# Kernel tuning notes

Measured on AMD Instinct MI355X. Metric: run time of the kernel, lower is better.

Reference implementation:

```python
import jax, jax.numpy as jnp
import numpy as np

DIM = 16      # must equal K*K per the module's reshape structure
K = 4         # kernel_size
HEADS = 8
SCALE = (DIM // HEADS) ** (-0.5)


def setup_inputs() -> dict:
    key = jax.random.key(0)
    k1, k2 = jax.random.split(key)
    x = jax.random.normal(k1, (2, 64, 67, 67), dtype=jnp.float32)
    # torch Linear(dim, 3*dim, bias=False) weight: [3*dim, dim]
    w_qkv = jax.random.normal(k2, (3 * DIM, DIM), dtype=jnp.float32) * 0.1
    return {"x": x, "w_qkv": w_qkv}


def reference(x, w_qkv):
    B, C, H, W = x.shape
    k = K
    Ho, Wo = H - k + 1, W - k + 1          # unfold output grid (stride=1)
    L = Ho * Wo
    # Unfold: patches[b, c, i*k+j, ph, pw] = x[b, c, ph+i, pw+j]
    # (matches torch F.unfold channel ordering c-major, then i, then j)
    patches = jnp.stack(
        [x[:, :, i:i + Ho, j:j + Wo] for i in range(k) for j in range(k)],
        axis=2,
    )  # [B, C, k*k, Ho, Wo]
    seq = L // (k * k)                      # L must be divisible by k*k
    # [B*C*k*k, seq, k*k] -- flatten (Ho,Wo)->L row-major then split into (seq, k*k)
    xu = patches.reshape(B * C * k * k, seq, k * k)
    # tiny attention over each row; feature dim = k*k = DIM
    qkv = xu @ w_qkv.T                      # [N, seq, 3*DIM]
    q, kk_, v = jnp.split(qkv, 3, axis=-1)
    scores = jnp.einsum('nqd,nkd->nqk', q, kk_) * SCALE   # [N, seq, seq]
    attn = jax.nn.softmax(scores, axis=-1)                # dropout = identity (eval)
    ao = jnp.einsum('nqk,nkd->nqd', attn, v)              # [N, seq, DIM]
    ao = ao.reshape(B, C, k, k, Ho, Wo)
    # overlap-add fold back onto the HxW grid
    out = jnp.zeros_like(x)
    for i in range(k):
        for j in range(k):
            out = out.at[:, :, i:Ho + i, j:Wo + j].add(ao[:, :, i, j])
    return out
```

## Files before the change

### kernel.cpp

```cpp
#include <hip/hip_runtime.h>


#define BATCH 2
#define CHAN 64
#define HWDIM 67
#define SEQ 256
#define DIM 16
#define NSEQ 2048
#define PLANE 4096
#define OUT_TOTAL (BATCH * CHAN * HWDIM * HWDIM)
#define ATT_SCALE 0.70710678118654752f
#define LOG2E 1.44269504088896340736f
#define HTILES 17

typedef _Float16 half4 __attribute__((ext_vector_type(4)));
typedef _Float16 half8 __attribute__((ext_vector_type(8)));
typedef float float4v __attribute__((ext_vector_type(4)));
typedef __fp16 fp16x2 __attribute__((ext_vector_type(2)));
typedef unsigned int uint2v __attribute__((ext_vector_type(2)));

static __device__ __forceinline__ half4 mk_half4(float a, float b, float c, float d) {
    fp16x2 lo = __builtin_amdgcn_cvt_pkrtz(a, b);
    fp16x2 hi = __builtin_amdgcn_cvt_pkrtz(c, d);
    uint2v u;
    u[0] = __builtin_bit_cast(unsigned int, lo);
    u[1] = __builtin_bit_cast(unsigned int, hi);
    return __builtin_bit_cast(half4, u);
}

static __device__ __forceinline__ half4 pack4(float4v c) {
    return mk_half4(c[0], c[1], c[2], c[3]);
}

static __device__ __forceinline__ void att_step(const half4 vf, const float4v sfr,
                                                float& l, float4v& oacc) {
    const float p0 = __builtin_amdgcn_exp2f(sfr[0]);
    const float p1 = __builtin_amdgcn_exp2f(sfr[1]);
    const float p2 = __builtin_amdgcn_exp2f(sfr[2]);
    const float p3 = __builtin_amdgcn_exp2f(sfr[3]);
    l += (p0 + p1) + (p2 + p3);
    const half4 pb = mk_half4(p0, p1, p2, p3);
    oacc = __builtin_amdgcn_mfma_f32_16x16x16f16(vf, pb, oacc, 0, 0, 0);
}

__global__ __launch_bounds__(512, 6) void ska_attn_pass1(
    const float* __restrict__ x,
    const float* __restrict__ w,
    _Float16* __restrict__ ao)
{
    __shared__ __align__(16) _Float16 buf[16][64][8];

    const int n = (int)(blockIdx.x & 7) * 256 + (int)(blockIdx.x >> 3);

    const int p  = n & 15;
    const int bc = n >> 4;
    const int oi = p >> 2;
    const int oj = p & 3;

    const int tid  = threadIdx.x;
    const int wave = tid >> 6;
    const int lane = tid & 63;
    const int o = lane & 15;
    const int g = lane >> 4;

    const float4 wq4 = *(const float4*)(w + ( 0 + o) * DIM + 4 * g);
    const float4 wk4 = *(const float4*)(w + (16 + o) * DIM + 4 * g);
    const float4 wv4 = *(const float4*)(w + (32 + o) * DIM + 4 * g);
    const half4 wqf = mk_half4(wq4.x * (ATT_SCALE * LOG2E), wq4.y * (ATT_SCALE * LOG2E),
                               wq4.z * (ATT_SCALE * LOG2E), wq4.w * (ATT_SCALE * LOG2E));
    const half4 wkf = mk_half4(wk4.x, wk4.y, wk4.z, wk4.w);
    const half4 wvf = mk_half4(wv4.x, wv4.y, wv4.z, wv4.w);

    const float4v zf = (float4v){0.f, 0.f, 0.f, 0.f};

    const int rowbase = bc * (HWDIM * HWDIM) + oi * HWDIM + oj;
    const int col = (o & 3) * 16 + 4 * g;
    half4 qfr[2];
#pragma unroll
    for (int u = 0; u < 2; ++u) {
        const int t = 2 * wave + u;
        const float* xp = x + rowbase + (4 * t + (o >> 2)) * HWDIM + col;
        const half4 xf = mk_half4(xp[0], xp[1], xp[2], xp[3]);
        const half4 kf = pack4(__builtin_amdgcn_mfma_f32_16x16x16f16(wkf, xf, zf, 0, 0, 0));
        const half4 vf = pack4(__builtin_amdgcn_mfma_f32_16x16x16f16(xf, wvf, zf, 0, 0, 0));
        const half8 kv = __builtin_shufflevector(kf, vf, 0, 1, 2, 3, 4, 5, 6, 7);
        *(half8*)&buf[t][lane][0] = kv;
        qfr[u] = pack4(__builtin_amdgcn_mfma_f32_16x16x16f16(wqf, xf, zf, 0, 0, 0));
    }
    __syncthreads();

    float4v oacc0 = zf, oacc1 = zf;
    float l0 = 0.f, l1 = 0.f;

    half8 kvc = *(const half8*)&buf[0][lane][0];
#pragma unroll 4
    for (int t = 0; t < 16; ++t) {
        const half8 kvn = *(const half8*)&buf[(t + 1) & 15][lane][0];
        const half4 kf = __builtin_shufflevector(kvc, kvc, 0, 1, 2, 3);
        const half4 vf = __builtin_shufflevector(kvc, kvc, 4, 5, 6, 7);
        const float4v s0 = __builtin_amdgcn_mfma_f32_16x16x16f16(kf, qfr[0], zf, 0, 0, 0);
        const float4v s1 = __builtin_amdgcn_mfma_f32_16x16x16f16(kf, qfr[1], zf, 0, 0, 0);
        att_step(vf, s0, l0, oacc0);
        att_step(vf, s1, l1, oacc1);
        kvc = kvn;
    }

#pragma unroll
    for (int j = 0; j < 2; ++j) {
        float lj = j ? l1 : l0;
        lj += __shfl_xor(lj, 16, 64);
        lj += __shfl_xor(lj, 32, 64);
        const float rl = __builtin_amdgcn_rcpf(lj);
        const float4v oa = j ? oacc1 : oacc0;
        const int query = (2 * wave + j) * 16 + o;
        const half4 hv = mk_half4(oa[0] * rl, oa[1] * rl,
                                  oa[2] * rl, oa[3] * rl);
        *(half4*)(ao + (size_t)n * PLANE + query * DIM + 4 * g) = hv;
    }
}

__global__ __launch_bounds__(256) void ska_fold_pass2(
    const _Float16* __restrict__ ao,
    float* __restrict__ out)
{
    __shared__ __align__(16) _Float16 sA[16][4][64];

    const int blk = (int)(blockIdx.x & 7) * 272 + (int)(blockIdx.x >> 3);
    const int h0  = (blk % HTILES) * 4;
    const int bc  = blk / HTILES;
    const int tid = threadIdx.x;

    {
        const int pl = tid >> 4;
        const int hh = (tid >> 2) & 3;
        const int pw = (tid & 3) * 16;
        const int i  = pl >> 2;
        const int prow = h0 + hh - i;
        half8 v0, v1;
        if (prow >= 0 && prow < 64) {
            const _Float16* src = ao + ((size_t)(bc * 16 + pl)) * PLANE + prow * 64 + pw;
            v0 = *(const half8*)src;
            v1 = *(const half8*)(src + 8);
        } else {
            const half8 z = (half8)(_Float16)0.f;
            v0 = z; v1 = z;
        }
        *(half8*)&sA[pl][hh][pw]     = v0;
        *(half8*)&sA[pl][hh][pw + 8] = v1;
    }
    __syncthreads();

    for (int px = tid; px < 4 * HWDIM; px += 256) {
        const int hh = px / HWDIM;
        const int ww = px % HWDIM;
        const int h  = h0 + hh;
        if (h >= HWDIM) continue;
        float acc = 0.f;
#pragma unroll
        for (int i = 0; i < 4; ++i) {
#pragma unroll
            for (int j = 0; j < 4; ++j) {
                const int pw = ww - j;
                if (pw < 0 || pw >= 64) continue;
                acc += (float)sA[i * 4 + j][hh][pw];
            }
        }
        out[((size_t)bc * HWDIM + h) * HWDIM + ww] = acc;
    }
}

__global__ __launch_bounds__(256) void ska_attn_atomic(
    const float* __restrict__ x, const float* __restrict__ w,
    float* __restrict__ out)
{
    __shared__ float sw[3 * DIM * DIM];
    __shared__ float sk[SEQ][DIM];
    __shared__ float sv[SEQ][DIM];

    const int n = blockIdx.x, p = n & 15, bc = n >> 4, oi = p >> 2, oj = p & 3;
    const int s = threadIdx.x, ph = s >> 2, pw0 = (s & 3) * DIM;

#pragma unroll
    for (int r = 0; r < 3; ++r) sw[r * 256 + s] = w[r * 256 + s];

    const float* xrow = x + ((size_t)bc * HWDIM + (ph + oi)) * HWDIM + pw0 + oj;
    float xr[DIM];
#pragma unroll
    for (int d = 0; d < DIM; ++d) xr[d] = xrow[d];
    __syncthreads();

    float q[DIM];
#pragma unroll
    for (int o = 0; o < DIM; ++o) {
        float aq = 0.f, ak = 0.f, av = 0.f;
#pragma unroll
        for (int d = 0; d < DIM; ++d) {
            aq += xr[d] * sw[o * DIM + d];
            ak += xr[d] * sw[(DIM + o) * DIM + d];
            av += xr[d] * sw[(2 * DIM + o) * DIM + d];
        }
        q[o] = aq * ATT_SCALE; sk[s][o] = ak; sv[s][o] = av;
    }
    __syncthreads();

    float l = 0.f, acc[DIM];
#pragma unroll
    for (int d = 0; d < DIM; ++d) acc[d] = 0.f;
    for (int t = 0; t < SEQ; ++t) {
        float sc = 0.f;
#pragma unroll
        for (int d = 0; d < DIM; ++d) sc += q[d] * sk[t][d];
        const float pe = __expf(sc);
        l += pe;
#pragma unroll
        for (int d = 0; d < DIM; ++d) acc[d] += pe * sv[t][d];
    }
    const float rl = 1.f / l;
    float* obase = out + ((size_t)bc * HWDIM + (ph + oi)) * HWDIM + pw0 + oj;
#pragma unroll
    for (int d = 0; d < DIM; ++d) atomicAdd(&obase[d], acc[d] * rl);
}

extern "C" void kernel_launch(void* const* d_in, const int* in_sizes, int n_in,
                              void* d_out, int out_size, void* d_ws, size_t ws_size,
                              hipStream_t stream) {
    const float* x = (const float*)d_in[0];
    const float* w = (const float*)d_in[1];
    float* out = (float*)d_out;

    const size_t need = (size_t)NSEQ * PLANE * sizeof(_Float16);
    if (ws_size >= need) {
        _Float16* ao = (_Float16*)d_ws;
        ska_attn_pass1<<<NSEQ, 512, 0, stream>>>(x, w, ao);
        ska_fold_pass2<<<BATCH * CHAN * HTILES, 256, 0, stream>>>(ao, out);
    } else {
        (void)hipMemsetAsync(out, 0, (size_t)out_size * sizeof(float), stream);
        ska_attn_atomic<<<NSEQ, 256, 0, stream>>>(x, w, out);
    }
}
```

Measured before the change: 88.89 us.

## Process four oj sequences per block with double-buffered K/V and prefetched x rows

Each pass-1 block now handles the four sequences that share the same (bc, oi) and differ only by column offset oj, looping over them instead of launching one block per sequence. The x loads for the next sequence are issued before the attention loop, and K/V go into a double-buffered shared array, so one barrier per iteration suffices and global load latency can overlap the MFMA work. Grid size drops by four and the launch bound's minimum-blocks hint goes from 6 to 2. The trade-off is fewer blocks for latency hiding, twice the shared memory per block, and longer serial work per block.

```diff
diff --git a/kernel.cpp b/kernel.cpp
--- a/kernel.cpp
+++ b/kernel.cpp
@@ -43,19 +43,17 @@
     oacc = __builtin_amdgcn_mfma_f32_16x16x16f16(vf, pb, oacc, 0, 0, 0);
 }
 
-__global__ __launch_bounds__(512, 6) void ska_attn_pass1(
+__global__ __launch_bounds__(512, 2) void ska_attn_pass1(
     const float* __restrict__ x,
     const float* __restrict__ w,
     _Float16* __restrict__ ao)
 {
-    __shared__ __align__(16) _Float16 buf[16][64][8];
-
-    const int n = (int)(blockIdx.x & 7) * 256 + (int)(blockIdx.x >> 3);
-
-    const int p  = n & 15;
-    const int bc = n >> 4;
-    const int oi = p >> 2;
-    const int oj = p & 3;
+    __shared__ __align__(16) _Float16 buf[2][16][64][8];
+
+    const int b  = (int)(blockIdx.x & 7) * 64 + (int)(blockIdx.x >> 3);
+    const int bc = b >> 2;
+    const int oi = b & 3;
+    const int n0 = bc * 16 + oi * 4;
 
     const int tid  = threadIdx.x;
     const int wave = tid >> 6;
@@ -73,49 +71,74 @@
 
     const float4v zf = (float4v){0.f, 0.f, 0.f, 0.f};
 
-    const int rowbase = bc * (HWDIM * HWDIM) + oi * HWDIM + oj;
-    const int col = (o & 3) * 16 + 4 * g;
-    half4 qfr[2];
-#pragma unroll
-    for (int u = 0; u < 2; ++u) {
-        const int t = 2 * wave + u;
-        const float* xp = x + rowbase + (4 * t + (o >> 2)) * HWDIM + col;
-        const half4 xf = mk_half4(xp[0], xp[1], xp[2], xp[3]);
-        const half4 kf = pack4(__builtin_amdgcn_mfma_f32_16x16x16f16(wkf, xf, zf, 0, 0, 0));
-        const half4 vf = pack4(__builtin_amdgcn_mfma_f32_16x16x16f16(xf, wvf, zf, 0, 0, 0));
-        const half8 kv = __builtin_shufflevector(kf, vf, 0, 1, 2, 3, 4, 5, 6, 7);
-        *(half8*)&buf[t][lane][0] = kv;
-        qfr[u] = pack4(__builtin_amdgcn_mfma_f32_16x16x16f16(wqf, xf, zf, 0, 0, 0));
-    }
-    __syncthreads();
-
-    float4v oacc0 = zf, oacc1 = zf;
-    float l0 = 0.f, l1 = 0.f;
-
-    half8 kvc = *(const half8*)&buf[0][lane][0];
+    const float* xb = x + ((size_t)bc * HWDIM + oi) * HWDIM + (o & 3) * 16 + 4 * g;
+    const int roff0 = (8 * wave + (o >> 2)) * HWDIM;
+    const int roff1 = roff0 + 4 * HWDIM;
+
+    float xr0a = xb[roff0 + 0], xr0b = xb[roff0 + 1],
+          xr0c = xb[roff0 + 2], xr0d = xb[roff0 + 3];
+    float xr1a = xb[roff1 + 0], xr1b = xb[roff1 + 1],
+          xr1c = xb[roff1 + 2], xr1d = xb[roff1 + 3];
+
+    for (int sq = 0; sq < 4; ++sq) {
+        const int cur = sq & 1;
+
+        half4 qfr0, qfr1;
+        {
+            const half4 xf0 = mk_half4(xr0a, xr0b, xr0c, xr0d);
+            const half4 kf0 = pack4(__builtin_amdgcn_mfma_f32_16x16x16f16(wkf, xf0, zf, 0, 0, 0));
+            const half4 vf0 = pack4(__builtin_amdgcn_mfma_f32_16x16x16f16(xf0, wvf, zf, 0, 0, 0));
+            *(half8*)&buf[cur][2 * wave][lane][0] =
+                __builtin_shufflevector(kf0, vf0, 0, 1, 2, 3, 4, 5, 6, 7);
+            qfr0 = pack4(__builtin_amdgcn_mfma_f32_16x16x16f16(wqf, xf0, zf, 0, 0, 0));
+
+            const half4 xf1 = mk_half4(xr1a, xr1b, xr1c, xr1d);
+            const half4 kf1 = pack4(__builtin_amdgcn_mfma_f32_16x16x16f16(wkf, xf1, zf, 0, 0, 0));
+            const half4 vf1 = pack4(__builtin_amdgcn_mfma_f32_16x16x16f16(xf1, wvf, zf, 0, 0, 0));
+            *(half8*)&buf[cur][2 * wave + 1][lane][0] =
+                __builtin_shufflevector(kf1, vf1, 0, 1, 2, 3, 4, 5, 6, 7);
+            qfr1 = pack4(__builtin_amdgcn_mfma_f32_16x16x16f16(wqf, xf1, zf, 0, 0, 0));
+        }
+
+        if (sq < 3) {
+            const int d = sq + 1;
+            xr0a = xb[roff0 + d + 0]; xr0b = xb[roff0 + d + 1];
+            xr0c = xb[roff0 + d + 2]; xr0d = xb[roff0 + d + 3];
+            xr1a = xb[roff1 + d + 0]; xr1b = xb[roff1 + d + 1];
+            xr1c = xb[roff1 + d + 2]; xr1d = xb[roff1 + d + 3];
+        }
+
+        __syncthreads();
+
+        float4v oacc0 = zf, oacc1 = zf;
+        float l0 = 0.f, l1 = 0.f;
+
+        half8 kvc = *(const half8*)&buf[cur][0][lane][0];
 #pragma unroll 4
-    for (int t = 0; t < 16; ++t) {
-        const half8 kvn = *(const half8*)&buf[(t + 1) & 15][lane][0];
-        const half4 kf = __builtin_shufflevector(kvc, kvc, 0, 1, 2, 3);
-        const half4 vf = __builtin_shufflevector(kvc, kvc, 4, 5, 6, 7);
-        const float4v s0 = __builtin_amdgcn_mfma_f32_16x16x16f16(kf, qfr[0], zf, 0, 0, 0);
-        const float4v s1 = __builtin_amdgcn_mfma_f32_16x16x16f16(kf, qfr[1], zf, 0, 0, 0);
-        att_step(vf, s0, l0, oacc0);
-        att_step(vf, s1, l1, oacc1);
-        kvc = kvn;
-    }
-
-#pragma unroll
-    for (int j = 0; j < 2; ++j) {
-        float lj = j ? l1 : l0;
-        lj += __shfl_xor(lj, 16, 64);
-        lj += __shfl_xor(lj, 32, 64);
-        const float rl = __builtin_amdgcn_rcpf(lj);
-        const float4v oa = j ? oacc1 : oacc0;
-        const int query = (2 * wave + j) * 16 + o;
-        const half4 hv = mk_half4(oa[0] * rl, oa[1] * rl,
-                                  oa[2] * rl, oa[3] * rl);
-        *(half4*)(ao + (size_t)n * PLANE + query * DIM + 4 * g) = hv;
+        for (int t = 0; t < 16; ++t) {
+            const half8 kvn = *(const half8*)&buf[cur][(t + 1) & 15][lane][0];
+            const half4 kf = __builtin_shufflevector(kvc, kvc, 0, 1, 2, 3);
+            const half4 vf = __builtin_shufflevector(kvc, kvc, 4, 5, 6, 7);
+            const float4v s0 = __builtin_amdgcn_mfma_f32_16x16x16f16(kf, qfr0, zf, 0, 0, 0);
+            const float4v s1 = __builtin_amdgcn_mfma_f32_16x16x16f16(kf, qfr1, zf, 0, 0, 0);
+            att_step(vf, s0, l0, oacc0);
+            att_step(vf, s1, l1, oacc1);
+            kvc = kvn;
+        }
+
+        const int n = n0 + sq;
+#pragma unroll
+        for (int j = 0; j < 2; ++j) {
+            float lj = j ? l1 : l0;
+            lj += __shfl_xor(lj, 16, 64);
+            lj += __shfl_xor(lj, 32, 64);
+            const float rl = __builtin_amdgcn_rcpf(lj);
+            const float4v oa = j ? oacc1 : oacc0;
+            const int query = (2 * wave + j) * 16 + o;
+            const half4 hv = mk_half4(oa[0] * rl, oa[1] * rl,
+                                      oa[2] * rl, oa[3] * rl);
+            *(half4*)(ao + (size_t)n * PLANE + query * DIM + 4 * g) = hv;
+        }
     }
 }
 
@@ -231,7 +254,7 @@
     const size_t need = (size_t)NSEQ * PLANE * sizeof(_Float16);
     if (ws_size >= need) {
         _Float16* ao = (_Float16*)d_ws;
-        ska_attn_pass1<<<NSEQ, 512, 0, stream>>>(x, w, ao);
+        ska_attn_pass1<<<NSEQ / 4, 512, 0, stream>>>(x, w, ao);
         ska_fold_pass2<<<BATCH * CHAN * HTILES, 256, 0, stream>>>(ao, out);
     } else {
         (void)hipMemsetAsync(out, 0, (size_t)out_size * sizeof(float), stream);
```

After: 91.37 us. +2.8%, slower.

## Fuse attention and overlap-add fold into one kernel per channel plane

Applied to the files above, without the earlier changes.

Replaces the two-pass pipeline (attention writing fp16 outputs to workspace, then a separate fold kernel) with a single kernel per (batch, channel) plane. Each of 16 waves handles one unfold offset, keeps all K/Q/V fragments in registers, and accumulates normalized outputs into a shared-memory fold buffer with LDS atomics before writing the plane. This removes the global intermediate round trip and a launch. In exchange, the grid shrinks to 128 large blocks, leaving many CUs idle, and register pressure per wave rises.

```diff
diff --git a/kernel.cpp b/kernel.cpp
--- a/kernel.cpp
+++ b/kernel.cpp
@@ -6,12 +6,8 @@
 #define HWDIM 67
 #define SEQ 256
 #define DIM 16
-#define NSEQ 2048
-#define PLANE 4096
-#define OUT_TOTAL (BATCH * CHAN * HWDIM * HWDIM)
 #define ATT_SCALE 0.70710678118654752f
 #define LOG2E 1.44269504088896340736f
-#define HTILES 17
 
 typedef _Float16 half4 __attribute__((ext_vector_type(4)));
 typedef _Float16 half8 __attribute__((ext_vector_type(8)));
@@ -43,22 +39,24 @@
     oacc = __builtin_amdgcn_mfma_f32_16x16x16f16(vf, pb, oacc, 0, 0, 0);
 }
 
-__global__ __launch_bounds__(512, 6) void ska_attn_pass1(
+__global__ __launch_bounds__(1024, 1) void ska_fused(
     const float* __restrict__ x,
     const float* __restrict__ w,
-    _Float16* __restrict__ ao)
+    float* __restrict__ out)
 {
-    __shared__ __align__(16) _Float16 buf[16][64][8];
+    __shared__ float fold[HWDIM][68];
 
-    const int n = (int)(blockIdx.x & 7) * 256 + (int)(blockIdx.x >> 3);
+    const int bc  = blockIdx.x;
+    const int tid = threadIdx.x;
 
-    const int p  = n & 15;
-    const int bc = n >> 4;
-    const int oi = p >> 2;
-    const int oj = p & 3;
+    {
+        float* ff = &fold[0][0];
+        for (int i = tid; i < HWDIM * 68; i += 1024) ff[i] = 0.f;
+    }
 
-    const int tid  = threadIdx.x;
-    const int wave = tid >> 6;
+    const int wv   = tid >> 6;
+    const int ii   = wv >> 2;
+    const int jj   = wv & 3;
     const int lane = tid & 63;
     const int o = lane & 15;
     const int g = lane >> 4;
@@ -73,152 +71,52 @@
 
     const float4v zf = (float4v){0.f, 0.f, 0.f, 0.f};
 
-    const int rowbase = bc * (HWDIM * HWDIM) + oi * HWDIM + oj;
-    const int col = (o & 3) * 16 + 4 * g;
-    half4 qfr[2];
+    const float* xb = x + ((size_t)bc * HWDIM + ii) * HWDIM + (o & 3) * 16 + 4 * g + jj;
+    half4 kf[16], vf[16], qf[16];
 #pragma unroll
-    for (int u = 0; u < 2; ++u) {
-        const int t = 2 * wave + u;
-        const float* xp = x + rowbase + (4 * t + (o >> 2)) * HWDIM + col;
+    for (int t = 0; t < 16; ++t) {
+        const float* xp = xb + (4 * t + (o >> 2)) * HWDIM;
         const half4 xf = mk_half4(xp[0], xp[1], xp[2], xp[3]);
-        const half4 kf = pack4(__builtin_amdgcn_mfma_f32_16x16x16f16(wkf, xf, zf, 0, 0, 0));
-        const half4 vf = pack4(__builtin_amdgcn_mfma_f32_16x16x16f16(xf, wvf, zf, 0, 0, 0));
-        const half8 kv = __builtin_shufflevector(kf, vf, 0, 1, 2, 3, 4, 5, 6, 7);
-        *(half8*)&buf[t][lane][0] = kv;
-        qfr[u] = pack4(__builtin_amdgcn_mfma_f32_16x16x16f16(wqf, xf, zf, 0, 0, 0));
+        kf[t] = pack4(__builtin_amdgcn_mfma_f32_16x16x16f16(wkf, xf, zf, 0, 0, 0));
+        vf[t] = pack4(__builtin_amdgcn_mfma_f32_16x16x16f16(xf, wvf, zf, 0, 0, 0));
+        qf[t] = pack4(__builtin_amdgcn_mfma_f32_16x16x16f16(wqf, xf, zf, 0, 0, 0));
     }
+
     __syncthreads();
 
-    float4v oacc0 = zf, oacc1 = zf;
-    float l0 = 0.f, l1 = 0.f;
-
-    half8 kvc = *(const half8*)&buf[0][lane][0];
-#pragma unroll 4
-    for (int t = 0; t < 16; ++t) {
-        const half8 kvn = *(const half8*)&buf[(t + 1) & 15][lane][0];
-        const half4 kf = __builtin_shufflevector(kvc, kvc, 0, 1, 2, 3);
-        const half4 vf = __builtin_shufflevector(kvc, kvc, 4, 5, 6, 7);
-        const float4v s0 = __builtin_amdgcn_mfma_f32_16x16x16f16(kf, qfr[0], zf, 0, 0, 0);
-        const float4v s1 = __builtin_amdgcn_mfma_f32_16x16x16f16(kf, qfr[1], zf, 0, 0, 0);
-        att_step(vf, s0, l0, oacc0);
-        att_step(vf, s1, l1, oacc1);
-        kvc = kvn;
+#pragma unroll
+    for (int jq = 0; jq < 16; jq += 2) {
+        float4v oacc0 = zf, oacc1 = zf;
+        float l0 = 0.f, l1 = 0.f;
+#pragma unroll
+        for (int t = 0; t < 16; ++t) {
+            const float4v s0 = __builtin_amdgcn_mfma_f32_16x16x16f16(kf[t], qf[jq],     zf, 0, 0, 0);
+            const float4v s1 = __builtin_amdgcn_mfma_f32_16x16x16f16(kf[t], qf[jq + 1], zf, 0, 0, 0);
+            att_step(vf[t], s0, l0, oacc0);
+            att_step(vf[t], s1, l1, oacc1);
+        }
+#pragma unroll
+        for (int u = 0; u < 2; ++u) {
+            float lj = u ? l1 : l0;
+            lj += __shfl_xor(lj, 16, 64);
+            lj += __shfl_xor(lj, 32, 64);
+            const float rl = __builtin_amdgcn_rcpf(lj);
+            const float4v oa = u ? oacc1 : oacc0;
+            const int r = 4 * (jq + u) + (o >> 2) + ii;
+            const int c = 16 * (o & 3) + 4 * g + jj;
+            atomicAdd(&fold[r][c + 0], oa[0] * rl);
+            atomicAdd(&fold[r][c + 1], oa[1] * rl);
+            atomicAdd(&fold[r][c + 2], oa[2] * rl);
+            atomicAdd(&fold[r][c + 3], oa[3] * rl);
+        }
     }
 
-#pragma unroll
-    for (int j = 0; j < 2; ++j) {
-        float lj = j ? l1 : l0;
-        lj += __shfl_xor(lj, 16, 64);
-        lj += __shfl_xor(lj, 32, 64);
-        const float rl = __builtin_amdgcn_rcpf(lj);
-        const float4v oa = j ? oacc1 : oacc0;
-        const int query = (2 * wave + j) * 16 + o;
-        const half4 hv = mk_half4(oa[0] * rl, oa[1] * rl,
-                                  oa[2] * rl, oa[3] * rl);
-        *(half4*)(ao + (size_t)n * PLANE + query * DIM + 4 * g) = hv;
-    }
-}
-
-__global__ __launch_bounds__(256) void ska_fold_pass2(
-    const _Float16* __restrict__ ao,
-    float* __restrict__ out)
-{
-    __shared__ __align__(16) _Float16 sA[16][4][64];
-
-    const int blk = (int)(blockIdx.x & 7) * 272 + (int)(blockIdx.x >> 3);
-    const int h0  = (blk % HTILES) * 4;
-    const int bc  = blk / HTILES;
-    const int tid = threadIdx.x;
-
-    {
-        const int pl = tid >> 4;
-        const int hh = (tid >> 2) & 3;
-        const int pw = (tid & 3) * 16;
-        const int i  = pl >> 2;
-        const int prow = h0 + hh - i;
-        half8 v0, v1;
-        if (prow >= 0 && prow < 64) {
-            const _Float16* src = ao + ((size_t)(bc * 16 + pl)) * PLANE + prow * 64 + pw;
-            v0 = *(const half8*)src;
-            v1 = *(const half8*)(src + 8);
-        } else {
-            const half8 z = (half8)(_Float16)0.f;
-            v0 = z; v1 = z;
-        }
-        *(half8*)&sA[pl][hh][pw]     = v0;
-        *(half8*)&sA[pl][hh][pw + 8] = v1;
-    }
     __syncthreads();
 
-    for (int px = tid; px < 4 * HWDIM; px += 256) {
-        const int hh = px / HWDIM;
-        const int ww = px % HWDIM;
-        const int h  = h0 + hh;
-        if (h >= HWDIM) continue;
-        float acc = 0.f;
-#pragma unroll
-        for (int i = 0; i < 4; ++i) {
-#pragma unroll
-            for (int j = 0; j < 4; ++j) {
-                const int pw = ww - j;
-                if (pw < 0 || pw >= 64) continue;
-                acc += (float)sA[i * 4 + j][hh][pw];
-            }
-        }
-        out[((size_t)bc * HWDIM + h) * HWDIM + ww] = acc;
+    float* ob = out + (size_t)bc * (HWDIM * HWDIM);
+    for (int pix = tid; pix < HWDIM * HWDIM; pix += 1024) {
+        ob[pix] = fold[pix / HWDIM][pix % HWDIM];
     }
-}
-
-__global__ __launch_bounds__(256) void ska_attn_atomic(
-    const float* __restrict__ x, const float* __restrict__ w,
-    float* __restrict__ out)
-{
-    __shared__ float sw[3 * DIM * DIM];
-    __shared__ float sk[SEQ][DIM];
-    __shared__ float sv[SEQ][DIM];
-
-    const int n = blockIdx.x, p = n & 15, bc = n >> 4, oi = p >> 2, oj = p & 3;
-    const int s = threadIdx.x, ph = s >> 2, pw0 = (s & 3) * DIM;
-
-#pragma unroll
-    for (int r = 0; r < 3; ++r) sw[r * 256 + s] = w[r * 256 + s];
-
-    const float* xrow = x + ((size_t)bc * HWDIM + (ph + oi)) * HWDIM + pw0 + oj;
-    float xr[DIM];
-#pragma unroll
-    for (int d = 0; d < DIM; ++d) xr[d] = xrow[d];
-    __syncthreads();
-
-    float q[DIM];
-#pragma unroll
-    for (int o = 0; o < DIM; ++o) {
-        float aq = 0.f, ak = 0.f, av = 0.f;
-#pragma unroll
-        for (int d = 0; d < DIM; ++d) {
-            aq += xr[d] * sw[o * DIM + d];
-            ak += xr[d] * sw[(DIM + o) * DIM + d];
-            av += xr[d] * sw[(2 * DIM + o) * DIM + d];
-        }
-        q[o] = aq * ATT_SCALE; sk[s][o] = ak; sv[s][o] = av;
-    }
-    __syncthreads();
-
-    float l = 0.f, acc[DIM];
-#pragma unroll
-    for (int d = 0; d < DIM; ++d) acc[d] = 0.f;
-    for (int t = 0; t < SEQ; ++t) {
-        float sc = 0.f;
-#pragma unroll
-        for (int d = 0; d < DIM; ++d) sc += q[d] * sk[t][d];
-        const float pe = __expf(sc);
-        l += pe;
-#pragma unroll
-        for (int d = 0; d < DIM; ++d) acc[d] += pe * sv[t][d];
-    }
-    const float rl = 1.f / l;
-    float* obase = out + ((size_t)bc * HWDIM + (ph + oi)) * HWDIM + pw0 + oj;
-#pragma unroll
-    for (int d = 0; d < DIM; ++d) atomicAdd(&obase[d], acc[d] * rl);
 }
 
 extern "C" void kernel_launch(void* const* d_in, const int* in_sizes, int n_in,
@@ -227,14 +125,7 @@
     const float* x = (const float*)d_in[0];
     const float* w = (const float*)d_in[1];
     float* out = (float*)d_out;
+    (void)d_ws; (void)ws_size; (void)in_sizes; (void)n_in; (void)out_size;
 
-    const size_t need = (size_t)NSEQ * PLANE * sizeof(_Float16);
-    if (ws_size >= need) {
-        _Float16* ao = (_Float16*)d_ws;
-        ska_attn_pass1<<<NSEQ, 512, 0, stream>>>(x, w, ao);
-        ska_fold_pass2<<<BATCH * CHAN * HTILES, 256, 0, stream>>>(ao, out);
-    } else {
-        (void)hipMemsetAsync(out, 0, (size_t)out_size * sizeof(float), stream);
-        ska_attn_atomic<<<NSEQ, 256, 0, stream>>>(x, w, out);
-    }
+    ska_fused<<<BATCH * CHAN, 1024, 0, stream>>>(x, w, out);
 }
```

Result: slower. 145.8 us (+64.0%).
